# Performance work log

Measured on AMD Instinct MI355X. Metric: run time of the kernel, lower is better.

The kernel has to match this reference:

```python
import jax, jax.numpy as jnp
import numpy as np

E = 16          # number of experts/gates accumulated so far
B = 32768       # batch of tokens
LATENT = 128    # latent_dim
HID = 64        # hidden_dim
CLASSES = 10


def setup_inputs() -> dict:
    key = jax.random.key(0)
    ks = jax.random.split(key, 8)
    x = jax.random.normal(ks[0], (B, 1, 28, 28), dtype=jnp.float32)
    # hard routing: each token assigned to exactly one expert (argmin of recon errors)
    assign = jax.random.randint(ks[1], (B,), 0, E)
    mask = (jnp.arange(E)[:, None] == assign[None, :])  # [E, B] bool, one-hot per column
    latent = jax.random.normal(ks[2], (E, B, LATENT), dtype=jnp.float32)
    s1 = 1.0 / np.sqrt(LATENT)
    s2 = 1.0 / np.sqrt(HID)
    W1 = jax.random.normal(ks[3], (E, LATENT, HID), dtype=jnp.float32) * s1
    b1 = jnp.zeros((E, HID), dtype=jnp.float32)
    W2 = jax.random.normal(ks[4], (E, HID, HID), dtype=jnp.float32) * s2
    b2 = jnp.zeros((E, HID), dtype=jnp.float32)
    W3 = jax.random.normal(ks[5], (E, HID, CLASSES), dtype=jnp.float32) * s2
    b3 = jnp.zeros((E, CLASSES), dtype=jnp.float32)
    return {"x": x, "mask": mask, "latent": latent,
            "W1": W1, "b1": b1, "W2": W2, "b2": b2, "W3": W3, "b3": b3}


def reference(x, mask, latent, W1, b1, W2, b2, W3, b3):
    # Each expert e sees its OWN latent representation latent[e]; the torch code
    # gathers masked rows, runs ExpertMLP_e, and scatters into a zero logits tensor.
    # With an exclusive (one-hot per token) mask this equals a masked sum of
    # per-expert outputs; unrouted tokens stay zero, matching torch.zeros init.
    h = jax.nn.relu(jnp.einsum('ebl,elh->ebh', latent, W1) + b1[:, None, :])
    h = jax.nn.relu(jnp.einsum('ebh,ehk->ebk', h, W2) + b2[:, None, :])
    out = jnp.einsum('ebh,ehc->ebc', h, W3) + b3[:, None, :]  # [E, B, C]
    logits = jnp.sum(jnp.where(mask[:, :, None], out, jnp.zeros((), out.dtype)), axis=0)
    return logits  # [B, CLASSES]
```

## Files before the change

kernel.cpp:

```cpp
#include <hip/hip_runtime.h>
#include <hip/hip_bf16.h>
#include <cstdint>
#include <cstddef>

#define NE 16
#define NB 32768
#define LATENT 128
#define HID 64
#define CLASSES 10
#define WPE 32

__global__ __launch_bounds__(256) void assign_kernel(
    const void* __restrict__ mask,
    int* __restrict__ counts,
    unsigned short* __restrict__ lists) {
    __shared__ int sMode;
    __shared__ int lCount[NE];
    __shared__ int gBase[NE];
    __shared__ unsigned short lList[NE][256];

    const int tid = threadIdx.x;
    if (tid == 0) sMode = 0;
    if (tid < NE) lCount[tid] = 0;
    __syncthreads();
    if (tid < 32) {
        const unsigned char* mb = (const unsigned char*)mask;
        int b = 1 + 4 * tid;
        int nz = 0;
        for (int e = 0; e < NE; ++e) nz |= mb[(size_t)e * NB + b];
        if (nz) atomicOr(&sMode, 1);
    }
    __syncthreads();
    const int mode = sMode;

    const int b = blockIdx.x * 256 + tid;
    int myE = 0;
    if (mode) {
        const unsigned char* m = (const unsigned char*)mask;
        for (int e = 0; e < NE; ++e)
            if (m[(size_t)e * NB + b]) { myE = e; break; }
    } else {
        const int* m = (const int*)mask;
        for (int e = 0; e < NE; ++e)
            if (m[(size_t)e * NB + b] != 0) { myE = e; break; }
    }
    int pos = atomicAdd(&lCount[myE], 1);
    lList[myE][pos] = (unsigned short)b;
    __syncthreads();

    if (tid < NE) gBase[tid] = atomicAdd(&counts[tid], lCount[tid]);
    __syncthreads();

    for (int e = 0; e < NE; ++e) {
        const int n = lCount[e], g0 = gBase[e];
        for (int i = tid; i < n; i += 256)
            lists[e * NB + g0 + i] = lList[e][i];
    }
}

__global__ __launch_bounds__(256) void expert_kernel(
    const float* __restrict__ latent,
    const float* __restrict__ W1, const float* __restrict__ b1,
    const float* __restrict__ W2, const float* __restrict__ b2,
    const float* __restrict__ W3, const float* __restrict__ b3,
    const int* __restrict__ counts,
    const unsigned short* __restrict__ lists,
    float* __restrict__ out)
{
    __shared__ float sX[LATENT * 64];

    const int e    = blockIdx.x / WPE;
    const int blk  = blockIdx.x % WPE;
    const int tid  = threadIdx.x;
    const int lane = tid & 63;
    const int jh   = __builtin_amdgcn_readfirstlane(tid >> 6);

    const int cnt = counts[e];
    const int ntiles = (cnt + 63) >> 6;
    const unsigned short* mylist = lists + e * NB;

    const float* w1e = W1 + (size_t)e * LATENT * HID + jh * 16;
    const float* w2e = W2 + (size_t)e * HID * HID + jh * 16;
    const float* b1e = b1 + e * HID + jh * 16;
    const float* b2e = b2 + e * HID + jh * 16;
    const float* w3e = W3 + (size_t)e * HID * CLASSES + jh * 5;
    const float* b3e = b3 + e * CLASSES + jh * 5;

    for (int tile = blk; tile < ntiles; tile += WPE) {
        const int base = tile * 64;

        {
            const int s = lane, q = jh;
            int idx = base + s;
            if (idx >= cnt) idx = cnt - 1;
            const int tok = mylist[idx];
            const float4* src = (const float4*)
                (latent + ((size_t)e * NB + tok) * LATENT + q * 32);
            #pragma unroll
            for (int i = 0; i < 8; ++i) {
                float4 v = src[i];
                int l = q * 32 + i * 4;
                sX[(l + 0) * 64 + s] = v.x;
                sX[(l + 1) * 64 + s] = v.y;
                sX[(l + 2) * 64 + s] = v.z;
                sX[(l + 3) * 64 + s] = v.w;
            }
        }
        __syncthreads();

        float acc[16];
        #pragma unroll
        for (int j = 0; j < 16; ++j) acc[j] = b1e[j];
        #pragma unroll 4
        for (int l = 0; l < LATENT; ++l) {
            float x = sX[l * 64 + lane];
            const float* wr = w1e + l * HID;
            #pragma unroll
            for (int j = 0; j < 16; ++j) acc[j] = fmaf(x, wr[j], acc[j]);
        }
        __syncthreads();
        #pragma unroll
        for (int j = 0; j < 16; ++j)
            sX[(jh * 16 + j) * 64 + lane] = fmaxf(acc[j], 0.f);
        __syncthreads();

        float acc2[16];
        #pragma unroll
        for (int j = 0; j < 16; ++j) acc2[j] = b2e[j];
        #pragma unroll 4
        for (int l = 0; l < HID; ++l) {
            float x = sX[l * 64 + lane];
            const float* wr = w2e + l * HID;
            #pragma unroll
            for (int j = 0; j < 16; ++j) acc2[j] = fmaf(x, wr[j], acc2[j]);
        }
        __syncthreads();
        #pragma unroll
        for (int j = 0; j < 16; ++j)
            sX[(jh * 16 + j) * 64 + lane] = fmaxf(acc2[j], 0.f);
        __syncthreads();

        if (jh < 2) {
            float a3[5];
            #pragma unroll
            for (int c = 0; c < 5; ++c) a3[c] = b3e[c];
            #pragma unroll 4
            for (int l = 0; l < HID; ++l) {
                float x = sX[l * 64 + lane];
                const float* wr = w3e + l * CLASSES;
                #pragma unroll
                for (int c = 0; c < 5; ++c) a3[c] = fmaf(x, wr[c], a3[c]);
            }
            int slot = base + lane;
            if (slot < cnt) {
                int tok = mylist[slot];
                float* o = out + (size_t)tok * CLASSES + jh * 5;
                #pragma unroll
                for (int c = 0; c < 5; ++c) o[c] = a3[c];
            }
        }
        __syncthreads();
    }
}

extern "C" void kernel_launch(void* const* d_in, const int* in_sizes, int n_in,
                              void* d_out, int out_size, void* d_ws, size_t ws_size,
                              hipStream_t stream) {
    const void*  mask   = d_in[1];
    const float* latent = (const float*)d_in[2];
    const float* W1 = (const float*)d_in[3];
    const float* b1 = (const float*)d_in[4];
    const float* W2 = (const float*)d_in[5];
    const float* b2 = (const float*)d_in[6];
    const float* W3 = (const float*)d_in[7];
    const float* b3 = (const float*)d_in[8];
    float* out = (float*)d_out;

    int* counts = (int*)d_ws;
    unsigned short* lists = (unsigned short*)((char*)d_ws + 128);

    hipMemsetAsync(d_ws, 0, 64, stream);
    assign_kernel<<<NB / 256, 256, 0, stream>>>(mask, counts, lists);
    expert_kernel<<<NE * WPE, 256, 0, stream>>>(latent, W1, b1, W2, b2, W3, b3,
                                                counts, lists, out);
}
```

Baseline: 406.4 us.

## Fuse token routing into expert kernel with per-block local mask scan

Removes the separate assign kernel, the workspace memset and the global per-expert token lists. Each block now reads its own expert's mask slice for a fixed 1024-token strip with vector loads and builds its token list in shared memory, then runs the MLP tiles from that list. This cuts two extra launches and the global scatter and gather of token indices. In exchange, how evenly work spreads across blocks now depends on how routed tokens fall within each strip, and the list order inside a block is set by atomic order.

```diff
diff --git a/kernel.cpp b/kernel.cpp
--- a/kernel.cpp
+++ b/kernel.cpp
@@ -1,5 +1,4 @@
 #include <hip/hip_runtime.h>
-#include <hip/hip_bf16.h>
 #include <cstdint>
 #include <cstddef>
 
@@ -9,75 +8,68 @@
 #define HID 64
 #define CLASSES 10
 #define WPE 32
+#define STRIP (NB / WPE)
 
-__global__ __launch_bounds__(256) void assign_kernel(
+__global__ __launch_bounds__(256) void fused_kernel(
     const void* __restrict__ mask,
-    int* __restrict__ counts,
-    unsigned short* __restrict__ lists) {
+    const float* __restrict__ latent,
+    const float* __restrict__ W1, const float* __restrict__ b1,
+    const float* __restrict__ W2, const float* __restrict__ b2,
+    const float* __restrict__ W3, const float* __restrict__ b3,
+    float* __restrict__ out)
+{
+    __shared__ float sX[LATENT * 64];
+    __shared__ unsigned short sList[STRIP];
+    __shared__ int sN;
     __shared__ int sMode;
-    __shared__ int lCount[NE];
-    __shared__ int gBase[NE];
-    __shared__ unsigned short lList[NE][256];
 
-    const int tid = threadIdx.x;
-    if (tid == 0) sMode = 0;
-    if (tid < NE) lCount[tid] = 0;
+    const int e    = blockIdx.x >> 5;
+    const int blk  = blockIdx.x & 31;
+    const int tid  = threadIdx.x;
+    const int lane = tid & 63;
+    const int jh   = __builtin_amdgcn_readfirstlane(tid >> 6);
+
+    if (tid == 0) { sN = 0; sMode = 0; }
     __syncthreads();
+
     if (tid < 32) {
         const unsigned char* mb = (const unsigned char*)mask;
         int b = 1 + 4 * tid;
         int nz = 0;
-        for (int e = 0; e < NE; ++e) nz |= mb[(size_t)e * NB + b];
+        #pragma unroll
+        for (int ee = 0; ee < NE; ++ee) nz |= mb[(size_t)ee * NB + b];
         if (nz) atomicOr(&sMode, 1);
     }
     __syncthreads();
-    const int mode = sMode;
 
-    const int b = blockIdx.x * 256 + tid;
-    int myE = 0;
-    if (mode) {
-        const unsigned char* m = (const unsigned char*)mask;
-        for (int e = 0; e < NE; ++e)
-            if (m[(size_t)e * NB + b]) { myE = e; break; }
+    const int tok0 = blk * STRIP;
+    if (sMode) {
+        const uchar4* m = (const uchar4*)((const unsigned char*)mask
+                                          + (size_t)e * NB + tok0);
+        uchar4 v = m[tid];
+        unsigned char c[4] = {v.x, v.y, v.z, v.w};
+        #pragma unroll
+        for (int k = 0; k < 4; ++k)
+            if (c[k]) {
+                int p = atomicAdd(&sN, 1);
+                sList[p] = (unsigned short)(tok0 + tid * 4 + k);
+            }
     } else {
-        const int* m = (const int*)mask;
-        for (int e = 0; e < NE; ++e)
-            if (m[(size_t)e * NB + b] != 0) { myE = e; break; }
+        const int4* m = (const int4*)((const int*)mask + (size_t)e * NB + tok0);
+        int4 v = m[tid];
+        int c[4] = {v.x, v.y, v.z, v.w};
+        #pragma unroll
+        for (int k = 0; k < 4; ++k)
+            if (c[k] != 0) {
+                int p = atomicAdd(&sN, 1);
+                sList[p] = (unsigned short)(tok0 + tid * 4 + k);
+            }
     }
-    int pos = atomicAdd(&lCount[myE], 1);
-    lList[myE][pos] = (unsigned short)b;
     __syncthreads();
 
-    if (tid < NE) gBase[tid] = atomicAdd(&counts[tid], lCount[tid]);
-    __syncthreads();
-
-    for (int e = 0; e < NE; ++e) {
-        const int n = lCount[e], g0 = gBase[e];
-        for (int i = tid; i < n; i += 256)
-            lists[e * NB + g0 + i] = lList[e][i];
-    }
-}
-
-__global__ __launch_bounds__(256) void expert_kernel(
-    const float* __restrict__ latent,
-    const float* __restrict__ W1, const float* __restrict__ b1,
-    const float* __restrict__ W2, const float* __restrict__ b2,
-    const float* __restrict__ W3, const float* __restrict__ b3,
-    const int* __restrict__ counts,
-    const unsigned short* __restrict__ lists,
-    float* __restrict__ out)
-{
-    __shared__ float sX[LATENT * 64];
-
-    const int e    = blockIdx.x / WPE;
-    const int blk  = blockIdx.x % WPE;
-    const int tid  = threadIdx.x;
-    const int lane = tid & 63;
-    const int jh   = __builtin_amdgcn_readfirstlane(tid >> 6);
-
-    const int cnt = counts[e];
+    const int cnt = sN;
+    if (cnt == 0) return;
     const int ntiles = (cnt + 63) >> 6;
-    const unsigned short* mylist = lists + e * NB;
 
     const float* w1e = W1 + (size_t)e * LATENT * HID + jh * 16;
     const float* w2e = W2 + (size_t)e * HID * HID + jh * 16;
@@ -86,14 +78,14 @@
     const float* w3e = W3 + (size_t)e * HID * CLASSES + jh * 5;
     const float* b3e = b3 + e * CLASSES + jh * 5;
 
-    for (int tile = blk; tile < ntiles; tile += WPE) {
+    for (int tile = 0; tile < ntiles; ++tile) {
         const int base = tile * 64;
 
         {
             const int s = lane, q = jh;
             int idx = base + s;
             if (idx >= cnt) idx = cnt - 1;
-            const int tok = mylist[idx];
+            const int tok = sList[idx];
             const float4* src = (const float4*)
                 (latent + ((size_t)e * NB + tok) * LATENT + q * 32);
             #pragma unroll
@@ -153,7 +145,7 @@
             }
             int slot = base + lane;
             if (slot < cnt) {
-                int tok = mylist[slot];
+                int tok = sList[slot];
                 float* o = out + (size_t)tok * CLASSES + jh * 5;
                 #pragma unroll
                 for (int c = 0; c < 5; ++c) o[c] = a3[c];
@@ -176,11 +168,8 @@
     const float* b3 = (const float*)d_in[8];
     float* out = (float*)d_out;
 
-    int* counts = (int*)d_ws;
-    unsigned short* lists = (unsigned short*)((char*)d_ws + 128);
+    (void)d_ws; (void)ws_size;
 
-    hipMemsetAsync(d_ws, 0, 64, stream);
-    assign_kernel<<<NB / 256, 256, 0, stream>>>(mask, counts, lists);
-    expert_kernel<<<NE * WPE, 256, 0, stream>>>(latent, W1, b1, W2, b2, W3, b3,
-                                                counts, lists, out);
+    fused_kernel<<<NE * WPE, 256, 0, stream>>>(mask, latent,
+                                               W1, b1, W2, b2, W3, b3, out);
 }
```

New measurement: 391.3 us. 1.04x faster.
